# Optimization experiments

Measured on AMD Instinct MI355X. Metric: run time of the kernel, lower is better.

## Reference

```python
import jax, jax.numpy as jnp
import numpy as np

# Static module config (matches init_kwargs)
K = 9            # kernel_size for piecewise-linear basis with kernel_shape (3,4)
GROUPS = 1
NLAT_IN, NLON_IN = 361, 720
NLAT_OUT, NLON_OUT = 181, 360
NNZ = 120000


def _disco_s2_contraction(x, ker_idx, row_idx, col_idx, vals):
    """Sparse DISCO contraction: y[b,c,k,ho,wo] = sum_e [ker_e=k][row_e=ho]
    vals_e * x[b,c,hi_e,(wi_e + wo*pscale) % nlon_in].
    Implemented as a longitude-roll scan with gather + segment_sum (no dense psi)."""
    B, C, Hi, Wi = x.shape
    pscale = Wi // NLON_OUT
    hi = col_idx // Wi          # [nnz] input latitude
    wi = col_idx % Wi           # [nnz] input longitude (unshifted)
    seg = ker_idx * NLAT_OUT + row_idx  # [nnz] output (k, ho) segment id

    def step(x_c, _):
        # gather all nnz entries for the current longitude shift: [nnz, B*C]
        g = x_c[:, :, hi, wi].reshape(B * C, -1).T
        y = jax.ops.segment_sum(g * vals[:, None], seg, num_segments=K * NLAT_OUT)
        # roll so next output longitude sees x[..., (wi + pscale) % Wi]
        return jnp.roll(x_c, -pscale, axis=-1), y

    _, ys = jax.lax.scan(step, x, None, length=NLON_OUT)  # [Wo, K*Ho, B*C]
    y = jnp.transpose(ys, (2, 1, 0)).reshape(B, C, K, NLAT_OUT, NLON_OUT)
    return y


def setup_inputs() -> dict:
    key = jax.random.key(0)
    k1, k2, k3, k4, k5, k6, k7 = jax.random.split(key, 7)
    B, Cin, Cout = 1, 32, 32
    x = jax.random.normal(k1, (B, Cin, NLAT_IN, NLON_IN), dtype=jnp.float32)
    psi_ker_idx = jax.random.randint(k2, (NNZ,), 0, K)
    psi_row_idx = jax.random.randint(k3, (NNZ,), 0, NLAT_OUT)
    psi_col_idx = jax.random.randint(k4, (NNZ,), 0, NLAT_IN * NLON_IN)
    psi_vals = jax.random.normal(k5, (NNZ,), dtype=jnp.float32) * 0.05
    groupsize = Cin // GROUPS
    scale = np.sqrt(1.0 / groupsize)
    weight = scale * jax.random.normal(k6, (Cout, groupsize, K), dtype=jnp.float32)
    bias = jax.random.normal(k7, (Cout,), dtype=jnp.float32) * 0.01
    return {"x": x, "psi_ker_idx": psi_ker_idx, "psi_row_idx": psi_row_idx,
            "psi_col_idx": psi_col_idx, "psi_vals": psi_vals,
            "weight": weight, "bias": bias}


def reference(x, psi_ker_idx, psi_row_idx, psi_col_idx, psi_vals, weight, bias):
    # sparse gather-weight-scatter contraction -> [B, C, K, Ho, Wo]
    xk = _disco_s2_contraction(x, psi_ker_idx, psi_row_idx, psi_col_idx, psi_vals)
    B, C, _, H, W = xk.shape
    groupsize = C // GROUPS
    xk = xk.reshape(B, GROUPS, groupsize, K, H, W)
    w = weight.reshape(GROUPS, -1, weight.shape[1], weight.shape[2])  # [g, o, c, k]
    out = jnp.einsum('bgckxy,gock->bgoxy', xk, w).reshape(B, -1, H, W)
    out = out + bias.reshape(1, -1, 1, 1)
    return out
```

## Files before the change

### kernel.cpp

```cpp
#include <hip/hip_runtime.h>
#include <hip/hip_bf16.h>
#include <stdint.h>

typedef uint32_t u32;
typedef unsigned short u16;
typedef float v2f __attribute__((ext_vector_type(2)));

#define NLAT_I 361
#define NLON_I 720
#define NLAT_O 181
#define NLON_O 360
#define KK 9
#define NNZ 120000
#define NSEG (KK * NLAT_O)
#define NPIX (NLAT_O * NLON_O)
#define NCH 32
#define SORT_CAP 512
#define ROWLEN 5760

#define NBLK1 233
#define SEGS_PER_BLK 7
#define NC 4
#define LDSCAP 160
#define SPIN_LIMIT 100

__device__ __forceinline__ u32 f2bf_rne(float f) {
    u32 b = __float_as_uint(f);
    return (b + 0x7FFFu + ((b >> 16) & 1u)) >> 16;
}

__device__ __forceinline__ int imin(int a, int b) { return a < b ? a : b; }

__global__ __launch_bounds__(256) void repack_kernel(const float* __restrict__ x,
                                                     u32* __restrict__ xp) {
    __shared__ u16 tile[32][732];
    int hi = blockIdx.x;
    int tid = threadIdx.x;
    const size_t plane = (size_t)NLAT_I * NLON_I;
#pragma unroll 1
    for (int c = 0; c < NCH; c++) {
        for (int col = tid; col < NLON_I; col += 256) {
            tile[c][col] = (u16)f2bf_rne(x[c * plane + (size_t)hi * NLON_I + col]);
        }
    }
    __syncthreads();
    for (int wdx = tid; wdx < 2 * ROWLEN; wdx += 256) {
        int p = wdx / ROWLEN;
        int rem = wdx - p * ROWLEN;
        int j = rem >> 4;
        int cp = rem & 15;
        int col = 2 * j + p;
        u32 v = (u32)tile[2 * cp][col] | ((u32)tile[2 * cp + 1][col] << 16);
        xp[(size_t)(2 * hi + p) * ROWLEN + rem] = v;
    }
}

__global__ __launch_bounds__(256) void hist_kernel(const int* __restrict__ ker,
                                                   const int* __restrict__ row,
                                                   int* __restrict__ counts) {
    int e = blockIdx.x * 256 + threadIdx.x;
    if (e >= NNZ) return;
    int seg = ker[e] * NLAT_O + row[e];
    atomicAdd(&counts[seg], 1);
}

__global__ __launch_bounds__(256) void scan_kernel(const int* __restrict__ counts,
                                                   int* __restrict__ offsets) {
    __shared__ int lsum[256];
    const int CH = 7;
    int t = threadIdx.x;
    int base = t * CH;
    int local[CH];
    int s = 0;
    for (int i = 0; i < CH; i++) {
        int v = (base + i < NSEG) ? counts[base + i] : 0;
        local[i] = s;
        s += v;
    }
    lsum[t] = s;
    __syncthreads();
    for (int off = 1; off < 256; off <<= 1) {
        int v = 0;
        if (t >= off) v = lsum[t - off];
        __syncthreads();
        if (t >= off) lsum[t] += v;
        __syncthreads();
    }
    int pre = (t == 0) ? 0 : lsum[t - 1];
    for (int i = 0; i < CH; i++) {
        if (base + i < NSEG) offsets[base + i] = pre + local[i];
    }
}

__global__ __launch_bounds__(256) void scatter_kernel(const int* __restrict__ ker,
                                                      const int* __restrict__ row,
                                                      const int* __restrict__ col,
                                                      const float* __restrict__ vals,
                                                      const int* __restrict__ offsets,
                                                      int* __restrict__ cursor,
                                                      int2* __restrict__ recs) {
    int e = blockIdx.x * 256 + threadIdx.x;
    if (e >= NNZ) return;
    int seg = ker[e] * NLAT_O + row[e];
    int pos = offsets[seg] + atomicAdd(&cursor[seg], 1);
    int c  = col[e];
    int hi = c / NLON_I;
    int wi = c % NLON_I;
    int p  = wi & 1;
    int a  = wi >> 1;
    u32 meta = ((u32)hi << 10) | ((u32)p << 9) | (u32)a;
    recs[pos] = make_int2((int)meta, __float_as_int(vals[e]));
}

__global__ __launch_bounds__(256) void sort_kernel(const int* __restrict__ offs,
                                                   const int* __restrict__ cnts,
                                                   int2* __restrict__ recs) {
    __shared__ u32 skey[SORT_CAP];
    __shared__ u32 sval[SORT_CAP];
    int s = blockIdx.x;
    int start = offs[s];
    int cnt = cnts[s];
    if (cnt > SORT_CAP) return;
    int t = threadIdx.x;
    for (int i = t; i < cnt; i += 256) {
        int2 r = recs[start + i];
        skey[i] = (u32)r.x;
        sval[i] = (u32)r.y;
    }
    __syncthreads();
    for (int i = t; i < cnt; i += 256) {
        u32 k = skey[i];
        int rank = 0;
        for (int j = 0; j < cnt; j++) {
            u32 kj = skey[j];
            rank += (kj < k || (kj == k && j < i)) ? 1 : 0;
        }
        recs[start + rank] = make_int2((int)k, (int)sval[i]);
    }
}


__device__ __forceinline__ v2f bf2(u32 u) {
    v2f r;
    r.x = __uint_as_float(u << 16);
    r.y = __uint_as_float(u & 0xFFFF0000u);
    return r;
}

__device__ __forceinline__ const uint4* entry_ptr(const u32* __restrict__ xph,
                                                  u32 m, int w) {
    int row = (int)(m >> 9);
    int a   = (int)(m & 0x1FF);
    int idx = a + w;
    idx = (idx >= NLON_O) ? idx - NLON_O : idx;
    return (const uint4*)(xph + ((size_t)(row * NLON_O + idx) << 4));
}

#define FMA8(q0, q1, vv, A)                 \
    {                                       \
        A[0] = bf2(q0.x) * vv + A[0];       \
        A[1] = bf2(q0.y) * vv + A[1];       \
        A[2] = bf2(q0.z) * vv + A[2];       \
        A[3] = bf2(q0.w) * vv + A[3];       \
        A[4] = bf2(q1.x) * vv + A[4];       \
        A[5] = bf2(q1.y) * vv + A[5];       \
        A[6] = bf2(q1.z) * vv + A[6];       \
        A[7] = bf2(q1.w) * vv + A[7];       \
    }

__device__ __forceinline__ void proc_range(const u32* __restrict__ xph,
                                           const int2* __restrict__ rec,
                                           int beg, int end, int w,
                                           v2f* __restrict__ A) {
    int i = beg;
#pragma unroll 1
    for (; i + 4 <= end; i += 4) {
        int2 r0 = rec[i];
        int2 r1 = rec[i + 1];
        int2 r2 = rec[i + 2];
        int2 r3 = rec[i + 3];
        const uint4* p0 = entry_ptr(xph, (u32)r0.x, w);
        const uint4* p1 = entry_ptr(xph, (u32)r1.x, w);
        const uint4* p2 = entry_ptr(xph, (u32)r2.x, w);
        const uint4* p3 = entry_ptr(xph, (u32)r3.x, w);
        uint4 a0 = p0[0]; uint4 a1 = p0[1];
        uint4 b0 = p1[0]; uint4 b1 = p1[1];
        uint4 c0 = p2[0]; uint4 c1 = p2[1];
        uint4 d0 = p3[0]; uint4 d1 = p3[1];
        v2f v0 = {__int_as_float(r0.y), __int_as_float(r0.y)};
        v2f v1 = {__int_as_float(r1.y), __int_as_float(r1.y)};
        v2f v2 = {__int_as_float(r2.y), __int_as_float(r2.y)};
        v2f v3 = {__int_as_float(r3.y), __int_as_float(r3.y)};
        FMA8(a0, a1, v0, A)
        FMA8(b0, b1, v1, A)
        FMA8(c0, c1, v2, A)
        FMA8(d0, d1, v3, A)
    }
#pragma unroll 1
    for (; i < end; ++i) {
        int2 r0 = rec[i];
        const uint4* p0 = entry_ptr(xph, (u32)r0.x, w);
        uint4 a0 = p0[0]; uint4 a1 = p0[1];
        v2f v0 = {__int_as_float(r0.y), __int_as_float(r0.y)};
        FMA8(a0, a1, v0, A)
    }
}

__global__ __launch_bounds__(768, 3) void stage1_kernel(const u32* __restrict__ xp,
                                                        const int* __restrict__ offs,
                                                        const int* __restrict__ cnts,
                                                        const int2* __restrict__ recs,
                                                        int* __restrict__ ctr,
                                                        u16* __restrict__ xk) {
    __shared__ int2 lrec[SEGS_PER_BLK][LDSCAP];
    __shared__ int scnt[SEGS_PER_BLK], soff[SEGS_PER_BLK];

    int b = blockIdx.x;
    int tid = threadIdx.x;

    if (tid < SEGS_PER_BLK) {
        int s = b * SEGS_PER_BLK + tid;
        int ok = (s < NSEG);
        scnt[tid] = ok ? cnts[s] : 0;
        soff[tid] = ok ? offs[s] : 0;
    }
    __syncthreads();

#pragma unroll
    for (int slot = 0; slot < SEGS_PER_BLK; slot++) {
        int c = imin(scnt[slot], LDSCAP);
        int o = soff[slot];
        for (int i = tid; i < c; i += 768) lrec[slot][i] = recs[o + i];
    }
    __syncthreads();

    int wo = tid >> 1, h = tid & 1;
    bool act = wo < NLON_O;
    int w = act ? wo : 0;
    const u32* xph = xp + h * 8;

    v2f acc[SEGS_PER_BLK][8];
#pragma unroll
    for (int slot = 0; slot < SEGS_PER_BLK; slot++)
#pragma unroll
        for (int j = 0; j < 8; j++) acc[slot][j] = (v2f){0.0f, 0.0f};

    for (int c = 0; c < NC; c++) {
#pragma unroll
        for (int slot = 0; slot < SEGS_PER_BLK; slot++) {
            int cnt = scnt[slot];
            int beg = (c * cnt) / NC;
            int end = ((c + 1) * cnt) / NC;
            if (end <= LDSCAP) {
                proc_range(xph, lrec[slot], beg, end, w, acc[slot]);
            } else {
                proc_range(xph, recs + soff[slot], beg, end, w, acc[slot]);
            }
        }
        if (c < NC - 1) {
            __syncthreads();
            if (tid == 0) {
                __hip_atomic_fetch_add(&ctr[c], 1, __ATOMIC_RELAXED,
                                       __HIP_MEMORY_SCOPE_AGENT);
                int spins = 0;
                while (spins < SPIN_LIMIT &&
                       __hip_atomic_load(&ctr[c], __ATOMIC_RELAXED,
                                         __HIP_MEMORY_SCOPE_AGENT) < (int)gridDim.x) {
                    __builtin_amdgcn_s_sleep(2);
                    ++spins;
                }
            }
            __syncthreads();
        }
    }

    if (act) {
#pragma unroll
        for (int slot = 0; slot < SEGS_PER_BLK; slot++) {
            int s = b * SEGS_PER_BLK + slot;
            if (s < NSEG) {
                int k = s / NLAT_O;
                int ho = s - k * NLAT_O;
                int pix = ho * NLON_O + wo;
#pragma unroll
                for (int j = 0; j < 8; j++) {
                    int ch = h * 16 + 2 * j;
                    xk[(size_t)(ch * KK + k) * NPIX + pix] =
                        (u16)f2bf_rne(acc[slot][j].x);
                    xk[(size_t)((ch + 1) * KK + k) * NPIX + pix] =
                        (u16)f2bf_rne(acc[slot][j].y);
                }
            }
        }
    }
}

#define S2_PP 64
#define S2_RPK 72

__global__ __launch_bounds__(256) void stage2_kernel(const u16* __restrict__ xk,
                                                     const float* __restrict__ W,
                                                     const float* __restrict__ bias,
                                                     float* __restrict__ out) {
    __shared__ float2 red[4][S2_PP][17];
    int pp  = threadIdx.x & 63;
    int ksl = threadIdx.x >> 6;
    int px2 = blockIdx.x * S2_PP + pp;
    bool act = px2 < NPIX / 2;
    int px = act ? px2 : 0;
    const u32* xk32 = (const u32*)xk;

    float a0[NCH], a1[NCH];
#pragma unroll
    for (int o = 0; o < NCH; o++) { a0[o] = 0.0f; a1[o] = 0.0f; }

    int rbase = ksl * S2_RPK;
#pragma unroll 4
    for (int rr = 0; rr < S2_RPK; rr++) {
        int r = rbase + rr;
        u32 u = xk32[(size_t)r * (NPIX / 2) + px];
        float x0 = __uint_as_float(u << 16);
        float x1 = __uint_as_float(u & 0xFFFF0000u);
#pragma unroll
        for (int o = 0; o < NCH; o++) {
            float wv = W[o * (NCH * KK) + r];
            a0[o] = fmaf(wv, x0, a0[o]);
            a1[o] = fmaf(wv, x1, a1[o]);
        }
    }

#pragma unroll 1
    for (int half = 0; half < 2; half++) {
        __syncthreads();
#pragma unroll
        for (int j = 0; j < 16; j++) {
            int o = half * 16 + j;
            red[ksl][pp][j] = make_float2(a0[o], a1[o]);
        }
        __syncthreads();
#pragma unroll
        for (int j = 0; j < 4; j++) {
            int oo = ksl * 4 + j;
            float2 s0 = red[0][pp][oo];
            float2 s1 = red[1][pp][oo];
            float2 s2 = red[2][pp][oo];
            float2 s3 = red[3][pp][oo];
            float sx = s0.x + s1.x + s2.x + s3.x;
            float sy = s0.y + s1.y + s2.y + s3.y;
            int o = half * 16 + oo;
            if (act) {
                float bv = bias[o];
                float2 v = make_float2(sx + bv, sy + bv);
                *(float2*)(out + (size_t)o * NPIX + 2 * px2) = v;
            }
        }
    }
}

extern "C" void kernel_launch(void* const* d_in, const int* in_sizes, int n_in,
                              void* d_out, int out_size, void* d_ws, size_t ws_size,
                              hipStream_t stream) {
    const float* x    = (const float*)d_in[0];
    const int* ker    = (const int*)d_in[1];
    const int* row    = (const int*)d_in[2];
    const int* col    = (const int*)d_in[3];
    const float* vals = (const float*)d_in[4];
    const float* W    = (const float*)d_in[5];
    const float* bias = (const float*)d_in[6];
    float* out        = (float*)d_out;

    char* ws = (char*)d_ws;
    const size_t off_xp   = 0;
    const size_t sz_xp    = (size_t)NLAT_I * 2 * ROWLEN * 4;
    const size_t off_cnt  = off_xp + sz_xp;
    const size_t off_off  = off_cnt + 6528;
    const size_t off_cur  = off_off + 6528;
    const size_t off_ctr  = off_cur + 6528;
    const size_t off_rec  = off_ctr + 64;
    const size_t off_xk   = off_rec + (size_t)NNZ * 8;

    u32* xp      = (u32*)(ws + off_xp);
    int* counts  = (int*)(ws + off_cnt);
    int* offsets = (int*)(ws + off_off);
    int* cursor  = (int*)(ws + off_cur);
    int* ctr     = (int*)(ws + off_ctr);
    int2* recs   = (int2*)(ws + off_rec);
    u16* xk      = (u16*)(ws + off_xk);

    hipMemsetAsync(ws + off_cnt, 0, 3 * 6528 + 64, stream);

    repack_kernel<<<NLAT_I, 256, 0, stream>>>(x, xp);
    hist_kernel<<<(NNZ + 255) / 256, 256, 0, stream>>>(ker, row, counts);
    scan_kernel<<<1, 256, 0, stream>>>(counts, offsets);
    scatter_kernel<<<(NNZ + 255) / 256, 256, 0, stream>>>(ker, row, col, vals,
                                                          offsets, cursor, recs);
    sort_kernel<<<NSEG, 256, 0, stream>>>(offsets, counts, recs);
    stage1_kernel<<<NBLK1, 768, 0, stream>>>(xp, offsets, counts, recs, ctr, xk);
    stage2_kernel<<<(NPIX / 2 + S2_PP - 1) / S2_PP, 256, 0, stream>>>(xk, W, bias, out);
}
```

Measured before the change: 339.3 us.

## Process stage1 segments sequentially with fewer per block and more blocks

Stage 1 now launches 512 blocks, each handling 3 or 4 segments one at a time, instead of 233 blocks each holding 7 segments' accumulators concurrently over 4 chunks. This cuts live accumulator registers from 7x8 to 8 vectors, which allows launch bounds of 6 blocks per CU for higher occupancy and latency hiding. The cross-block spin barrier now sits between segments rather than between chunks, and results are written after each segment. The trade-offs are that each block's loop over its segments is serial and the bounded spin waits on a larger grid.

```diff
diff --git a/kernel.cpp b/kernel.cpp
--- a/kernel.cpp
+++ b/kernel.cpp
@@ -18,9 +18,9 @@
 #define SORT_CAP 512
 #define ROWLEN 5760
 
-#define NBLK1 233
-#define SEGS_PER_BLK 7
-#define NC 4
+#define NBLK1 512
+#define MAXS 4
+#define RBLK 93
 #define LDSCAP 160
 #define SPIN_LIMIT 100
 
@@ -206,28 +206,30 @@
     }
 }
 
-__global__ __launch_bounds__(768, 3) void stage1_kernel(const u32* __restrict__ xp,
+__global__ __launch_bounds__(768, 6) void stage1_kernel(const u32* __restrict__ xp,
                                                         const int* __restrict__ offs,
                                                         const int* __restrict__ cnts,
                                                         const int2* __restrict__ recs,
                                                         int* __restrict__ ctr,
                                                         u16* __restrict__ xk) {
-    __shared__ int2 lrec[SEGS_PER_BLK][LDSCAP];
-    __shared__ int scnt[SEGS_PER_BLK], soff[SEGS_PER_BLK];
+    __shared__ int2 lrec[MAXS][LDSCAP];
+    __shared__ int scnt[MAXS], soff[MAXS];
 
     int b = blockIdx.x;
     int tid = threadIdx.x;
-
-    if (tid < SEGS_PER_BLK) {
-        int s = b * SEGS_PER_BLK + tid;
-        int ok = (s < NSEG);
+    int nb = 3 + ((b < RBLK) ? 1 : 0);
+    int start = b * 3 + ((b < RBLK) ? b : RBLK);
+
+    if (tid < MAXS) {
+        int s = start + tid;
+        int ok = (tid < nb) && (s < NSEG);
         scnt[tid] = ok ? cnts[s] : 0;
         soff[tid] = ok ? offs[s] : 0;
     }
     __syncthreads();
 
 #pragma unroll
-    for (int slot = 0; slot < SEGS_PER_BLK; slot++) {
+    for (int slot = 0; slot < MAXS; slot++) {
         int c = imin(scnt[slot], LDSCAP);
         int o = soff[slot];
         for (int i = tid; i < c; i += 768) lrec[slot][i] = recs[o + i];
@@ -239,58 +241,45 @@
     int w = act ? wo : 0;
     const u32* xph = xp + h * 8;
 
-    v2f acc[SEGS_PER_BLK][8];
-#pragma unroll
-    for (int slot = 0; slot < SEGS_PER_BLK; slot++)
-#pragma unroll
-        for (int j = 0; j < 8; j++) acc[slot][j] = (v2f){0.0f, 0.0f};
-
-    for (int c = 0; c < NC; c++) {
-#pragma unroll
-        for (int slot = 0; slot < SEGS_PER_BLK; slot++) {
-            int cnt = scnt[slot];
-            int beg = (c * cnt) / NC;
-            int end = ((c + 1) * cnt) / NC;
-            if (end <= LDSCAP) {
-                proc_range(xph, lrec[slot], beg, end, w, acc[slot]);
-            } else {
-                proc_range(xph, recs + soff[slot], beg, end, w, acc[slot]);
+#pragma unroll 1
+    for (int t = 0; t < MAXS; t++) {
+        v2f acc[8];
+#pragma unroll
+        for (int j = 0; j < 8; j++) acc[j] = (v2f){0.0f, 0.0f};
+
+        int cnt = scnt[t];
+        int lim = imin(cnt, LDSCAP);
+        proc_range(xph, lrec[t], 0, lim, w, acc);
+        if (cnt > LDSCAP)
+            proc_range(xph, recs + soff[t], LDSCAP, cnt, w, acc);
+
+        int s = start + t;
+        if (act && t < nb && s < NSEG) {
+            int k = s / NLAT_O;
+            int ho = s - k * NLAT_O;
+            int pix = ho * NLON_O + wo;
+#pragma unroll
+            for (int j = 0; j < 8; j++) {
+                int ch = h * 16 + 2 * j;
+                xk[(size_t)(ch * KK + k) * NPIX + pix] = (u16)f2bf_rne(acc[j].x);
+                xk[(size_t)((ch + 1) * KK + k) * NPIX + pix] = (u16)f2bf_rne(acc[j].y);
             }
         }
-        if (c < NC - 1) {
+
+        if (t < MAXS - 1) {
             __syncthreads();
             if (tid == 0) {
-                __hip_atomic_fetch_add(&ctr[c], 1, __ATOMIC_RELAXED,
+                __hip_atomic_fetch_add(&ctr[t], 1, __ATOMIC_RELAXED,
                                        __HIP_MEMORY_SCOPE_AGENT);
                 int spins = 0;
                 while (spins < SPIN_LIMIT &&
-                       __hip_atomic_load(&ctr[c], __ATOMIC_RELAXED,
+                       __hip_atomic_load(&ctr[t], __ATOMIC_RELAXED,
                                          __HIP_MEMORY_SCOPE_AGENT) < (int)gridDim.x) {
                     __builtin_amdgcn_s_sleep(2);
                     ++spins;
                 }
             }
             __syncthreads();
-        }
-    }
-
-    if (act) {
-#pragma unroll
-        for (int slot = 0; slot < SEGS_PER_BLK; slot++) {
-            int s = b * SEGS_PER_BLK + slot;
-            if (s < NSEG) {
-                int k = s / NLAT_O;
-                int ho = s - k * NLAT_O;
-                int pix = ho * NLON_O + wo;
-#pragma unroll
-                for (int j = 0; j < 8; j++) {
-                    int ch = h * 16 + 2 * j;
-                    xk[(size_t)(ch * KK + k) * NPIX + pix] =
-                        (u16)f2bf_rne(acc[slot][j].x);
-                    xk[(size_t)((ch + 1) * KK + k) * NPIX + pix] =
-                        (u16)f2bf_rne(acc[slot][j].y);
-                }
-            }
         }
     }
 }
```

New measurement: 492.8 us. 1.45x slower.

## Fuse histogram into repack kernel and move per-segment sort into stage1 LDS

Applied to the files above, without the earlier changes.

The histogram pass is folded into the repack launch as extra blocks, and the separate sort kernel is removed. The rank sort of each segment's records now runs inside stage1 on the copy already held in LDS, before accumulation starts. This saves two kernel launches and a global read/write pass over the records. In exchange, stage1 gains a serial per-slot rank sort with barriers. Segments larger than LDSCAP are no longer sorted in global memory, and in the old code any segment over 512 records was skipped anyway.

```diff
diff --git a/kernel.cpp b/kernel.cpp
--- a/kernel.cpp
+++ b/kernel.cpp
@@ -15,7 +15,6 @@
 #define NSEG (KK * NLAT_O)
 #define NPIX (NLAT_O * NLON_O)
 #define NCH 32
-#define SORT_CAP 512
 #define ROWLEN 5760
 
 #define NBLK1 233
@@ -24,6 +23,8 @@
 #define LDSCAP 160
 #define SPIN_LIMIT 100
 
+#define HIST_BLKS ((NNZ + 255) / 256)
+
 __device__ __forceinline__ u32 f2bf_rne(float f) {
     u32 b = __float_as_uint(f);
     return (b + 0x7FFFu + ((b >> 16) & 1u)) >> 16;
@@ -31,11 +32,22 @@
 
 __device__ __forceinline__ int imin(int a, int b) { return a < b ? a : b; }
 
-__global__ __launch_bounds__(256) void repack_kernel(const float* __restrict__ x,
-                                                     u32* __restrict__ xp) {
+__global__ __launch_bounds__(256) void repack_hist_kernel(const float* __restrict__ x,
+                                                          u32* __restrict__ xp,
+                                                          const int* __restrict__ ker,
+                                                          const int* __restrict__ row,
+                                                          int* __restrict__ counts) {
+    int tid = threadIdx.x;
+    if (blockIdx.x >= NLAT_I) {
+        int e = (blockIdx.x - NLAT_I) * 256 + tid;
+        if (e < NNZ) {
+            int seg = ker[e] * NLAT_O + row[e];
+            atomicAdd(&counts[seg], 1);
+        }
+        return;
+    }
     __shared__ u16 tile[32][732];
     int hi = blockIdx.x;
-    int tid = threadIdx.x;
     const size_t plane = (size_t)NLAT_I * NLON_I;
 #pragma unroll 1
     for (int c = 0; c < NCH; c++) {
@@ -53,15 +65,6 @@
         u32 v = (u32)tile[2 * cp][col] | ((u32)tile[2 * cp + 1][col] << 16);
         xp[(size_t)(2 * hi + p) * ROWLEN + rem] = v;
     }
-}
-
-__global__ __launch_bounds__(256) void hist_kernel(const int* __restrict__ ker,
-                                                   const int* __restrict__ row,
-                                                   int* __restrict__ counts) {
-    int e = blockIdx.x * 256 + threadIdx.x;
-    if (e >= NNZ) return;
-    int seg = ker[e] * NLAT_O + row[e];
-    atomicAdd(&counts[seg], 1);
 }
 
 __global__ __launch_bounds__(256) void scan_kernel(const int* __restrict__ counts,
@@ -110,33 +113,6 @@
     int a  = wi >> 1;
     u32 meta = ((u32)hi << 10) | ((u32)p << 9) | (u32)a;
     recs[pos] = make_int2((int)meta, __float_as_int(vals[e]));
-}
-
-__global__ __launch_bounds__(256) void sort_kernel(const int* __restrict__ offs,
-                                                   const int* __restrict__ cnts,
-                                                   int2* __restrict__ recs) {
-    __shared__ u32 skey[SORT_CAP];
-    __shared__ u32 sval[SORT_CAP];
-    int s = blockIdx.x;
-    int start = offs[s];
-    int cnt = cnts[s];
-    if (cnt > SORT_CAP) return;
-    int t = threadIdx.x;
-    for (int i = t; i < cnt; i += 256) {
-        int2 r = recs[start + i];
-        skey[i] = (u32)r.x;
-        sval[i] = (u32)r.y;
-    }
-    __syncthreads();
-    for (int i = t; i < cnt; i += 256) {
-        u32 k = skey[i];
-        int rank = 0;
-        for (int j = 0; j < cnt; j++) {
-            u32 kj = skey[j];
-            rank += (kj < k || (kj == k && j < i)) ? 1 : 0;
-        }
-        recs[start + rank] = make_int2((int)k, (int)sval[i]);
-    }
 }
 
 
@@ -234,6 +210,26 @@
     }
     __syncthreads();
 
+#pragma unroll 1
+    for (int slot = 0; slot < SEGS_PER_BLK; slot++) {
+        int cnt = imin(scnt[slot], LDSCAP);
+        int2 myrec;
+        int myrank = -1;
+        if (tid < cnt) {
+            myrec = lrec[slot][tid];
+            u32 k = (u32)myrec.x;
+            int rank = 0;
+            for (int j = 0; j < cnt; j++) {
+                u32 kj = (u32)lrec[slot][j].x;
+                rank += (kj < k || (kj == k && j < tid)) ? 1 : 0;
+            }
+            myrank = rank;
+        }
+        __syncthreads();
+        if (myrank >= 0) lrec[slot][myrank] = myrec;
+    }
+    __syncthreads();
+
     int wo = tid >> 1, h = tid & 1;
     bool act = wo < NLON_O;
     int w = act ? wo : 0;
@@ -389,12 +385,10 @@
 
     hipMemsetAsync(ws + off_cnt, 0, 3 * 6528 + 64, stream);
 
-    repack_kernel<<<NLAT_I, 256, 0, stream>>>(x, xp);
-    hist_kernel<<<(NNZ + 255) / 256, 256, 0, stream>>>(ker, row, counts);
+    repack_hist_kernel<<<NLAT_I + HIST_BLKS, 256, 0, stream>>>(x, xp, ker, row, counts);
     scan_kernel<<<1, 256, 0, stream>>>(counts, offsets);
-    scatter_kernel<<<(NNZ + 255) / 256, 256, 0, stream>>>(ker, row, col, vals,
-                                                          offsets, cursor, recs);
-    sort_kernel<<<NSEG, 256, 0, stream>>>(offsets, counts, recs);
+    scatter_kernel<<<HIST_BLKS, 256, 0, stream>>>(ker, row, col, vals,
+                                                  offsets, cursor, recs);
     stage1_kernel<<<NBLK1, 768, 0, stream>>>(xp, offsets, counts, recs, ctr, xk);
     stage2_kernel<<<(NPIX / 2 + S2_PP - 1) / S2_PP, 256, 0, stream>>>(xk, W, bias, out);
 }
```

After: 345.9 us. No clear change (+2.0%).
